# Performance work log

Measured on AMD Instinct MI355X. Metric: run time of the kernel, lower is better.

## Reference

```python
import jax, jax.numpy as jnp
import numpy as np

N, E = 50000, 800000
IN_DIM, HID, HEADS, NUM_CLASSES, NUM_GRAPHS, NUM_LAYERS = 64, 64, 4, 10000, 256, 3
OUT_W = HID * HEADS  # 256


def _gat_layer(x, src, dst, W, a_src, a_dst, b, n_nodes):
    # x: [N, in], W: [heads*out, in], a_src/a_dst: [heads, out], b: [heads*out]
    h = (x @ W.T).reshape(n_nodes, HEADS, HID)            # [N, H, D]
    s_src = jnp.einsum('nhd,hd->nh', h, a_src)            # [N, H]
    s_dst = jnp.einsum('nhd,hd->nh', h, a_dst)
    alpha = jax.nn.leaky_relu(s_src[src] + s_dst[dst], 0.2)  # [E, H]
    m = jax.ops.segment_max(alpha, dst, num_segments=n_nodes)
    m = jnp.where(jnp.isfinite(m), m, 0.0)                # isolated-node safety
    ex = jnp.exp(alpha - m[dst])
    denom = jax.ops.segment_sum(ex, dst, num_segments=n_nodes)
    w = ex / (denom[dst] + 1e-16)                         # PyG softmax epsilon
    out = jax.ops.segment_sum(h[src] * w[:, :, None], dst, num_segments=n_nodes)
    return out.reshape(n_nodes, HEADS * HID) + b


def setup_inputs() -> dict:
    key = jax.random.key(0)
    ks = jax.random.split(key, 20)
    inp = {
        'x': jax.random.normal(ks[0], (N, IN_DIM), jnp.float32),
        'edge_index': jax.random.randint(ks[1], (2, E), 0, N, jnp.int32),
        'batch': jnp.sort(jax.random.randint(ks[2], (N,), 0, NUM_GRAPHS, jnp.int32)),
        'class_label': jax.random.randint(ks[3], (NUM_GRAPHS,), 0, NUM_CLASSES, jnp.int32),
        'emb': jax.random.normal(ks[4], (NUM_CLASSES, HID), jnp.float32),
    }
    in_dims = [IN_DIM + HID, OUT_W, OUT_W]
    for l in range(NUM_LAYERS):
        kw = jax.random.split(ks[5 + l], 4)
        d_in = in_dims[l]
        sc = 1.0 / np.sqrt(d_in)
        inp[f'W{l}'] = jax.random.uniform(kw[0], (OUT_W, d_in), jnp.float32, -sc, sc)
        inp[f'asrc{l}'] = jax.random.uniform(kw[1], (HEADS, HID), jnp.float32, -sc, sc)
        inp[f'adst{l}'] = jax.random.uniform(kw[2], (HEADS, HID), jnp.float32, -sc, sc)
        inp[f'b{l}'] = jnp.zeros((OUT_W,), jnp.float32)
    sc = 1.0 / np.sqrt(OUT_W)
    inp['cls_W'] = jax.random.uniform(ks[10], (1, OUT_W), jnp.float32, -sc, sc)
    inp['cls_b'] = jnp.zeros((1,), jnp.float32)
    return inp


def reference(x, edge_index, batch, class_label, emb,
              W0, asrc0, adst0, b0,
              W1, asrc1, adst1, b1,
              W2, asrc2, adst2, b2,
              cls_W, cls_b):
    n = x.shape[0]
    # template embedding aligned per node
    t = emb[class_label][batch]                          # [N, HID]
    h = jnp.concatenate([x, t], axis=-1)                 # [N, IN+HID]
    # PyG GATConv adds self-loops by default
    loop = jnp.arange(n, dtype=edge_index.dtype)
    src = jnp.concatenate([edge_index[0], loop])
    dst = jnp.concatenate([edge_index[1], loop])
    params = [(W0, asrc0, adst0, b0), (W1, asrc1, adst1, b1), (W2, asrc2, adst2, b2)]
    for (W, a_s, a_d, b) in params:
        h = _gat_layer(h, src, dst, W, a_s, a_d, b, n)
        h = jax.nn.leaky_relu(h, 0.01)                   # F.leaky_relu default slope
    return h @ cls_W.T + cls_b                           # [N, 1]
```

## Files before the change

kernel.cpp:

```cpp
#include <hip/hip_runtime.h>
#include <hip/hip_fp16.h>
#include <math.h>

#define NNODES 50000
#define NEDGES 800000
#define NT_TILES (((NNODES + 127) / 128) * 2)
#define NGROUPS ((NNODES + 3) / 4)
#define NH0 (NNODES * 128)
#define NPREP4 (NH0 / 4 + 163840 / 4)

typedef __attribute__((ext_vector_type(8))) _Float16 f16x8;
typedef __attribute__((ext_vector_type(4))) _Float16 f16x4;
typedef __attribute__((ext_vector_type(4))) float f32x4;

static __device__ __forceinline__ void gl_lds16(const void* g, void* l) {
    __builtin_amdgcn_global_load_lds(
        (const __attribute__((address_space(1))) void*)g,
        (__attribute__((address_space(3))) void*)l, 16, 0, 0);
}

static __device__ __forceinline__ float sel4(float4 v, int head) {
    float r = v.x;
    r = (head == 1) ? v.y : r;
    r = (head == 2) ? v.z : r;
    r = (head == 3) ? v.w : r;
    return r;
}

__global__ void prep_kernel(const float* __restrict__ x,
                            const int* __restrict__ batch,
                            const int* __restrict__ class_label,
                            const float* __restrict__ emb,
                            const float* __restrict__ W0,
                            const float* __restrict__ W1,
                            const float* __restrict__ W2,
                            _Float16* __restrict__ h0,
                            _Float16* __restrict__ F0,
                            _Float16* __restrict__ F1,
                            _Float16* __restrict__ F2) {
    int i4 = blockIdx.x * blockDim.x + threadIdx.x;
    const int NH04 = NH0 / 4;
    if (i4 < NH04) {
        int idx = i4 * 4;
        int n = idx >> 7, c = idx & 127;
        float4 v;
        if (c < 64) v = *(const float4*)&x[(n << 6) + c];
        else        v = *(const float4*)&emb[class_label[batch[n]] * 64 + (c - 64)];
        f16x4 h = {(_Float16)v.x, (_Float16)v.y, (_Float16)v.z, (_Float16)v.w};
        *(f16x4*)&h0[idx] = h;
    } else if (i4 < NPREP4) {
        int i = (i4 - NH04) * 4;
        const float* src; _Float16* dst;
        if (i < 32768)       { src = W0 + i;           dst = F0 + i; }
        else if (i < 98304)  { src = W1 + (i - 32768); dst = F1 + (i - 32768); }
        else                 { src = W2 + (i - 98304); dst = F2 + (i - 98304); }
        float4 v = *(const float4*)src;
        f16x4 h = {(_Float16)v.x, (_Float16)v.y, (_Float16)v.z, (_Float16)v.w};
        *(f16x4*)dst = h;
    }
}

template <int K>
static __device__ void gemm_tile_dev(const _Float16* __restrict__ A,
                                     const _Float16* __restrict__ W,
                                     const float* __restrict__ a_src,
                                     const float* __restrict__ a_dst,
                                     _Float16* __restrict__ Cf,
                                     float* __restrict__ ssrc,
                                     float* __restrict__ sdst,
                                     char* smem, int bm, int bn) {
    _Float16* sA = (_Float16*)smem;
    _Float16* sB = (_Float16*)(smem + 16384);
    const int M = NNODES;
    int tid = threadIdx.x;
    int lane = tid & 63, wave = tid >> 6;
    int wm = wave >> 1, wn = wave & 1;
    int l16 = lane & 15, quad = lane >> 4;
    int rsub = lane >> 3;
    int kcs = (lane & 7) ^ rsub;
    int sw = l16 & 7;

    f32x4 acc[4][4];
#pragma unroll
    for (int r = 0; r < 4; ++r)
#pragma unroll
        for (int c = 0; c < 4; ++c) acc[r][c] = (f32x4){0.f, 0.f, 0.f, 0.f};

#pragma unroll
    for (int s = 0; s < K / 64; ++s) {
        int ks = s * 64;
        __syncthreads();
#pragma unroll
        for (int j = 0; j < 4; ++j) {
            int seg = wave * 4 + j;
            int r = seg * 8 + rsub;
            int acol = ks + kcs * 8;
            int garow = bm + r; if (garow > M - 1) garow = M - 1;
            gl_lds16(A + (size_t)garow * K + acol, &sA[seg * 512]);
            gl_lds16(W + (size_t)(bn + r) * K + acol, &sB[seg * 512]);
        }
        __syncthreads();
#pragma unroll
        for (int ks32 = 0; ks32 < 2; ++ks32) {
            f16x8 af[4], bf[4];
#pragma unroll
            for (int r = 0; r < 4; ++r) {
                int row = wm * 64 + r * 16 + l16;
                af[r] = *(const f16x8*)&sA[row * 64 + ((ks32 * 4 + quad) ^ sw) * 8];
            }
#pragma unroll
            for (int c = 0; c < 4; ++c) {
                int row = wn * 64 + c * 16 + l16;
                bf[c] = *(const f16x8*)&sB[row * 64 + ((ks32 * 4 + quad) ^ sw) * 8];
            }
#pragma unroll
            for (int r = 0; r < 4; ++r)
#pragma unroll
                for (int c = 0; c < 4; ++c)
                    acc[r][c] = __builtin_amdgcn_mfma_f32_16x16x32_f16(
                        bf[c], af[r], acc[r][c], 0, 0, 0);
        }
    }

    int headblk = (bn + wn * 64) >> 6;
    f32x4 av[4], dv[4];
#pragma unroll
    for (int c = 0; c < 4; ++c) {
        av[c] = *(const f32x4*)&a_src[headblk * 64 + c * 16 + quad * 4];
        dv[c] = *(const f32x4*)&a_dst[headblk * 64 + c * 16 + quad * 4];
    }
#pragma unroll
    for (int r = 0; r < 4; ++r) {
        int grow = bm + wm * 64 + r * 16 + l16;
        bool ok = grow < M;
        float ps = 0.f, pd = 0.f;
#pragma unroll
        for (int c = 0; c < 4; ++c) {
            f32x4 a = acc[r][c];
            ps += a[0] * av[c][0] + a[1] * av[c][1]
                + a[2] * av[c][2] + a[3] * av[c][3];
            pd += a[0] * dv[c][0] + a[1] * dv[c][1]
                + a[2] * dv[c][2] + a[3] * dv[c][3];
            if (ok) {
                f16x4 hv = {(_Float16)a[0], (_Float16)a[1],
                            (_Float16)a[2], (_Float16)a[3]};
                *(f16x4*)&Cf[(size_t)grow * 256 + bn + wn * 64 + c * 16 + quad * 4] = hv;
            }
        }
        ps += __shfl_xor(ps, 16, 64);
        ps += __shfl_xor(ps, 32, 64);
        pd += __shfl_xor(pd, 16, 64);
        pd += __shfl_xor(pd, 32, 64);
        if (quad == 0 && ok) {
            ssrc[grow * 4 + headblk] = ps;
            sdst[grow * 4 + headblk] = pd;
        }
    }
}

template <int K>
__global__ __launch_bounds__(256) void gemm_mfma_kernel(
        const _Float16* __restrict__ A, const _Float16* __restrict__ W,
        const float* __restrict__ a_src, const float* __restrict__ a_dst,
        _Float16* __restrict__ Cf,
        float* __restrict__ ssrc, float* __restrict__ sdst) {
    __shared__ __align__(16) char smem[32768];
    gemm_tile_dev<K>(A, W, a_src, a_dst, Cf, ssrc, sdst, smem,
                     blockIdx.x * 128, blockIdx.y * 128);
}

__global__ __launch_bounds__(256) void gemm0_bucket_kernel(
        const _Float16* __restrict__ A, const _Float16* __restrict__ W,
        const float* __restrict__ a_src, const float* __restrict__ a_dst,
        _Float16* __restrict__ Cf,
        float* __restrict__ ssrc, float* __restrict__ sdst,
        const int* __restrict__ ei,
        int* __restrict__ deg, int* __restrict__ slots) {
    __shared__ __align__(16) char smem[32768];
    int b = blockIdx.x;
    if ((b & 1) == 0) {
        int tile = b >> 1;
        if (tile < NT_TILES)
            gemm_tile_dev<128>(A, W, a_src, a_dst, Cf, ssrc, sdst, smem,
                               (tile >> 1) * 128, (tile & 1) * 128);
    } else {
        int rel = b >> 1;
        int stride = NT_TILES * 256;
        for (int e = rel * 256 + (int)threadIdx.x; e < NEDGES; e += stride) {
            int d = ei[NEDGES + e];
            int pos = atomicAdd(&deg[d], 1);
            if (pos < 64) slots[(size_t)d * 64 + pos] = ei[e];
        }
    }
}

template <bool LAST>
__global__ __launch_bounds__(256) void aggregate_kernel(
        const _Float16* __restrict__ hpf,
        const float* __restrict__ ssrc,
        const float* __restrict__ sdst,
        const int* __restrict__ deg,
        const int* __restrict__ slots,
        const float* __restrict__ bias,
        _Float16* __restrict__ out_h,
        const float* __restrict__ cls_W,
        const float* __restrict__ cls_b,
        float* __restrict__ out) {
    __shared__ __align__(16) float s_w[4][64][4];
    __shared__ int s_idx[4][64];
    int lane = threadIdx.x & 63;
    int slot = threadIdx.x >> 6;
    int n = blockIdx.x * 4 + slot;
    if (n >= NNODES) return;
    int head = lane >> 4;
    int dn = deg[n]; if (dn > 64) dn = 64;
    float4 sd = ((const float4*)sdst)[n];
    const f16x4* hp4 = (const f16x4*)hpf;

    float4 ssl = ((const float4*)ssrc)[n];
    float ax = ssl.x + sd.x, ay = ssl.y + sd.y;
    float az = ssl.z + sd.z, aw = ssl.w + sd.w;
    ax = ax > 0.f ? ax : 0.2f * ax;
    ay = ay > 0.f ? ay : 0.2f * ay;
    az = az > 0.f ? az : 0.2f * az;
    aw = aw > 0.f ? aw : 0.2f * aw;
    float4 exs = {__expf(ax), __expf(ay), __expf(az), __expf(aw)};
    float wself = sel4(exs, head);
    f16x4 vs = hp4[(size_t)n * 64 + lane];
    float dsum = wself;
    float4 acc = {wself * (float)vs.x, wself * (float)vs.y,
                  wself * (float)vs.z, wself * (float)vs.w};

    float4 ex = {0.f, 0.f, 0.f, 0.f};
    int s = 0;
    if (lane < dn) {
        s = slots[(size_t)n * 64 + lane];
        float4 ss = ((const float4*)ssrc)[s];
        float bx = ss.x + sd.x, by = ss.y + sd.y;
        float bz = ss.z + sd.z, bw = ss.w + sd.w;
        bx = bx > 0.f ? bx : 0.2f * bx;
        by = by > 0.f ? by : 0.2f * by;
        bz = bz > 0.f ? bz : 0.2f * bz;
        bw = bw > 0.f ? bw : 0.2f * bw;
        ex.x = __expf(bx); ex.y = __expf(by);
        ex.z = __expf(bz); ex.w = __expf(bw);
    }
    *(float4*)&s_w[slot][lane][0] = ex;
    s_idx[slot][lane] = s;

    int e = 0;
    for (; e + 8 <= dn; e += 8) {
        int si[8]; float w[8]; f16x4 v[8];
#pragma unroll
        for (int t = 0; t < 8; ++t) {
            si[t] = s_idx[slot][e + t];
            w[t] = s_w[slot][e + t][head];
        }
#pragma unroll
        for (int t = 0; t < 8; ++t) v[t] = hp4[(size_t)si[t] * 64 + lane];
#pragma unroll
        for (int t = 0; t < 8; ++t) {
            dsum += w[t];
            acc.x += w[t] * (float)v[t].x;
            acc.y += w[t] * (float)v[t].y;
            acc.z += w[t] * (float)v[t].z;
            acc.w += w[t] * (float)v[t].w;
        }
    }
    for (; e < dn; ++e) {
        int si = s_idx[slot][e];
        float w = s_w[slot][e][head];
        f16x4 v = hp4[(size_t)si * 64 + lane];
        dsum += w;
        acc.x += w * (float)v.x; acc.y += w * (float)v.y;
        acc.z += w * (float)v.z; acc.w += w * (float)v.w;
    }

    float inv = 1.f / (dsum + 1e-16f);
    float4 bv = ((const float4*)bias)[lane];
    float4 o;
    o.x = acc.x * inv + bv.x;
    o.y = acc.y * inv + bv.y;
    o.z = acc.z * inv + bv.z;
    o.w = acc.w * inv + bv.w;
    o.x = o.x > 0.f ? o.x : 0.01f * o.x;
    o.y = o.y > 0.f ? o.y : 0.01f * o.y;
    o.z = o.z > 0.f ? o.z : 0.01f * o.z;
    o.w = o.w > 0.f ? o.w : 0.01f * o.w;

    if (!LAST) {
        f16x4 ov = {(_Float16)o.x, (_Float16)o.y, (_Float16)o.z, (_Float16)o.w};
        ((f16x4*)out_h)[(size_t)n * 64 + lane] = ov;
    } else {
        float4 wv = ((const float4*)cls_W)[lane];
        float sdot = o.x * wv.x + o.y * wv.y + o.z * wv.z + o.w * wv.w;
#pragma unroll
        for (int off = 1; off < 64; off <<= 1)
            sdot += __shfl_xor(sdot, off, 64);
        if (lane == 0) out[n] = sdot + cls_b[0];
    }
}

extern "C" void kernel_launch(void* const* d_in, const int* in_sizes, int n_in,
                              void* d_out, int out_size, void* d_ws, size_t ws_size,
                              hipStream_t stream) {
    const float* x     = (const float*)d_in[0];
    const int*   ei    = (const int*)d_in[1];
    const int*   batch = (const int*)d_in[2];
    const int*   clab  = (const int*)d_in[3];
    const float* emb   = (const float*)d_in[4];
    const float* W[3]    = {(const float*)d_in[5], (const float*)d_in[9],  (const float*)d_in[13]};
    const float* asrc[3] = {(const float*)d_in[6], (const float*)d_in[10], (const float*)d_in[14]};
    const float* adst[3] = {(const float*)d_in[7], (const float*)d_in[11], (const float*)d_in[15]};
    const float* bias[3] = {(const float*)d_in[8], (const float*)d_in[12], (const float*)d_in[16]};
    const float* clsW = (const float*)d_in[17];
    const float* clsb = (const float*)d_in[18];
    float* out = (float*)d_out;

    char* ws = (char*)d_ws;
    size_t off = 0;
    auto alloc = [&](size_t bytes) {
        void* p = ws + off;
        off += (bytes + 255) & ~(size_t)255;
        return p;
    };
    _Float16* Cf   = (_Float16*)alloc((size_t)NNODES * 256 * 2);
    _Float16* hA   = (_Float16*)alloc((size_t)NNODES * 256 * 2);
    _Float16* h0f  = (_Float16*)alloc((size_t)NNODES * 128 * 2);
    _Float16* Wf[3];
    Wf[0] = (_Float16*)alloc((size_t)256 * 128 * 2);
    Wf[1] = (_Float16*)alloc((size_t)256 * 256 * 2);
    Wf[2] = (_Float16*)alloc((size_t)256 * 256 * 2);
    float* ssrc  = (float*)alloc((size_t)NNODES * 4 * 4);
    float* sdst  = (float*)alloc((size_t)NNODES * 4 * 4);
    int*   deg   = (int*)alloc((size_t)NNODES * 4);
    int*   slots = (int*)alloc((size_t)NNODES * 64 * 4);
    (void)ws_size; (void)in_sizes; (void)n_in; (void)out_size;

    hipMemsetAsync(deg, 0, (size_t)NNODES * 4, stream);

    prep_kernel<<<dim3((NPREP4 + 255) / 256), dim3(256), 0, stream>>>(
        x, batch, clab, emb, W[0], W[1], W[2], h0f, Wf[0], Wf[1], Wf[2]);

    dim3 gemm_grid((NNODES + 127) / 128, 2);
    dim3 node_grid(NGROUPS);

    gemm0_bucket_kernel<<<dim3(NT_TILES * 2), dim3(256), 0, stream>>>(
        h0f, Wf[0], asrc[0], adst[0], Cf, ssrc, sdst, ei, deg, slots);
    aggregate_kernel<false><<<node_grid, dim3(256), 0, stream>>>(
        Cf, ssrc, sdst, deg, slots, bias[0], hA, nullptr, nullptr, nullptr);

    gemm_mfma_kernel<256><<<gemm_grid, dim3(256), 0, stream>>>(
        hA, Wf[1], asrc[1], adst[1], Cf, ssrc, sdst);
    aggregate_kernel<false><<<node_grid, dim3(256), 0, stream>>>(
        Cf, ssrc, sdst, deg, slots, bias[1], hA, nullptr, nullptr, nullptr);

    gemm_mfma_kernel<256><<<gemm_grid, dim3(256), 0, stream>>>(
        hA, Wf[2], asrc[2], adst[2], Cf, ssrc, sdst);
    aggregate_kernel<true><<<node_grid, dim3(256), 0, stream>>>(
        Cf, ssrc, sdst, deg, slots, bias[2], nullptr, clsW, clsb, out);
}
```

Measured before the change: 377.0 us.

## Double-buffer GEMM LDS tiles and fold degree zeroing into prep kernel

The GEMM main loop now uses two LDS buffers, issuing global-to-LDS loads for the next K-slice before computing the current one, so memory latency overlaps with MFMA work and one barrier per step is removed. Shared memory per block doubles to 64 KB, which may lower occupancy. The separate hipMemsetAsync for the degree array is replaced by extra threads in prep_kernel that zero it, removing one launch. For K=128 there are only two stages, so the overlap gain is limited.

Measured after the change: 373.4 us (median of 2 runs). Within noise of the previous version (-1.0%).

```diff
diff --git a/kernel.cpp b/kernel.cpp
--- a/kernel.cpp
+++ b/kernel.cpp
@@ -7,7 +7,10 @@
 #define NT_TILES (((NNODES + 127) / 128) * 2)
 #define NGROUPS ((NNODES + 3) / 4)
 #define NH0 (NNODES * 128)
-#define NPREP4 (NH0 / 4 + 163840 / 4)
+#define NH04 (NH0 / 4)
+#define NW4 (163840 / 4)
+#define NDEG4 (NNODES / 4)
+#define NPREP4 (NH04 + NW4 + NDEG4)
 
 typedef __attribute__((ext_vector_type(8))) _Float16 f16x8;
 typedef __attribute__((ext_vector_type(4))) _Float16 f16x4;
@@ -37,9 +40,9 @@
                             _Float16* __restrict__ h0,
                             _Float16* __restrict__ F0,
                             _Float16* __restrict__ F1,
-                            _Float16* __restrict__ F2) {
+                            _Float16* __restrict__ F2,
+                            int* __restrict__ deg) {
     int i4 = blockIdx.x * blockDim.x + threadIdx.x;
-    const int NH04 = NH0 / 4;
     if (i4 < NH04) {
         int idx = i4 * 4;
         int n = idx >> 7, c = idx & 127;
@@ -48,7 +51,7 @@
         else        v = *(const float4*)&emb[class_label[batch[n]] * 64 + (c - 64)];
         f16x4 h = {(_Float16)v.x, (_Float16)v.y, (_Float16)v.z, (_Float16)v.w};
         *(f16x4*)&h0[idx] = h;
-    } else if (i4 < NPREP4) {
+    } else if (i4 < NH04 + NW4) {
         int i = (i4 - NH04) * 4;
         const float* src; _Float16* dst;
         if (i < 32768)       { src = W0 + i;           dst = F0 + i; }
@@ -57,6 +60,10 @@
         float4 v = *(const float4*)src;
         f16x4 h = {(_Float16)v.x, (_Float16)v.y, (_Float16)v.z, (_Float16)v.w};
         *(f16x4*)dst = h;
+    } else if (i4 < NPREP4) {
+        int j = (i4 - NH04 - NW4) * 4;
+        int4 z = {0, 0, 0, 0};
+        *(int4*)&deg[j] = z;
     }
 }
 
@@ -69,8 +76,6 @@
                                      float* __restrict__ ssrc,
                                      float* __restrict__ sdst,
                                      char* smem, int bm, int bn) {
-    _Float16* sA = (_Float16*)smem;
-    _Float16* sB = (_Float16*)(smem + 16384);
     const int M = NNODES;
     int tid = threadIdx.x;
     int lane = tid & 63, wave = tid >> 6;
@@ -86,20 +91,29 @@
 #pragma unroll
         for (int c = 0; c < 4; ++c) acc[r][c] = (f32x4){0.f, 0.f, 0.f, 0.f};
 
-#pragma unroll
-    for (int s = 0; s < K / 64; ++s) {
+    const int NST = K / 64;
+    auto issue = [&](int buf, int s) {
+        _Float16* dA = (_Float16*)(smem + buf * 32768);
+        _Float16* dB = (_Float16*)(smem + buf * 32768 + 16384);
         int ks = s * 64;
-        __syncthreads();
 #pragma unroll
         for (int j = 0; j < 4; ++j) {
             int seg = wave * 4 + j;
             int r = seg * 8 + rsub;
             int acol = ks + kcs * 8;
             int garow = bm + r; if (garow > M - 1) garow = M - 1;
-            gl_lds16(A + (size_t)garow * K + acol, &sA[seg * 512]);
-            gl_lds16(W + (size_t)(bn + r) * K + acol, &sB[seg * 512]);
-        }
-        __syncthreads();
+            gl_lds16(A + (size_t)garow * K + acol, &dA[seg * 512]);
+            gl_lds16(W + (size_t)(bn + r) * K + acol, &dB[seg * 512]);
+        }
+    };
+
+    issue(0, 0);
+    __syncthreads();
+#pragma unroll
+    for (int s = 0; s < NST; ++s) {
+        if (s + 1 < NST) issue((s + 1) & 1, s + 1);
+        const _Float16* sA = (const _Float16*)(smem + (s & 1) * 32768);
+        const _Float16* sB = (const _Float16*)(smem + (s & 1) * 32768 + 16384);
 #pragma unroll
         for (int ks32 = 0; ks32 < 2; ++ks32) {
             f16x8 af[4], bf[4];
@@ -120,6 +134,7 @@
                     acc[r][c] = __builtin_amdgcn_mfma_f32_16x16x32_f16(
                         bf[c], af[r], acc[r][c], 0, 0, 0);
         }
+        __syncthreads();
     }
 
     int headblk = (bn + wn * 64) >> 6;
@@ -164,7 +179,7 @@
         const float* __restrict__ a_src, const float* __restrict__ a_dst,
         _Float16* __restrict__ Cf,
         float* __restrict__ ssrc, float* __restrict__ sdst) {
-    __shared__ __align__(16) char smem[32768];
+    __shared__ __align__(16) char smem[65536];
     gemm_tile_dev<K>(A, W, a_src, a_dst, Cf, ssrc, sdst, smem,
                      blockIdx.x * 128, blockIdx.y * 128);
 }
@@ -176,7 +191,7 @@
         float* __restrict__ ssrc, float* __restrict__ sdst,
         const int* __restrict__ ei,
         int* __restrict__ deg, int* __restrict__ slots) {
-    __shared__ __align__(16) char smem[32768];
+    __shared__ __align__(16) char smem[65536];
     int b = blockIdx.x;
     if ((b & 1) == 0) {
         int tile = b >> 1;
@@ -337,10 +352,8 @@
     int*   slots = (int*)alloc((size_t)NNODES * 64 * 4);
     (void)ws_size; (void)in_sizes; (void)n_in; (void)out_size;
 
-    hipMemsetAsync(deg, 0, (size_t)NNODES * 4, stream);
-
     prep_kernel<<<dim3((NPREP4 + 255) / 256), dim3(256), 0, stream>>>(
-        x, batch, clab, emb, W[0], W[1], W[2], h0f, Wf[0], Wf[1], Wf[2]);
+        x, batch, clab, emb, W[0], W[1], W[2], h0f, Wf[0], Wf[1], Wf[2], deg);
 
     dim3 gemm_grid((NNODES + 127) / 128, 2);
     dim3 node_grid(NGROUPS);
```
